# Optimization experiments

Measured on AMD Instinct MI355X. Metric: run time of the kernel, lower is better.

## Reference

```python
import jax, jax.numpy as jnp
import numpy as np

B, L, D = 1, 1024, 1024
NL = 4            # n_layers
N = 16            # d_state
DI = 2 * D        # d_inner (expand=2)
DTR = (D + 15) // 16  # dt_rank = ceil(d_model/16) = 64
K = 4             # depthwise conv kernel size
EPS = 1e-5


def setup_inputs() -> dict:
    key = jax.random.key(0)
    ks = jax.random.split(key, 8)
    s = lambda k, shp, sc: jax.random.normal(k, shp, jnp.float32) * sc
    x = s(ks[0], (B, L, D), 1.0)
    norm_w = jnp.ones((NL, D), jnp.float32)
    in_w = s(ks[1], (NL, 2 * DI, D), D ** -0.5)          # in_proj (no bias)
    conv_w = s(ks[2], (NL, DI, K), 0.5)                   # depthwise conv1d weight
    conv_b = s(ks[3], (NL, DI), 0.02)                     # conv1d bias
    xproj_w = s(ks[4], (NL, DTR + 2 * N, DI), DI ** -0.5) # x_proj (no bias)
    dt_w = s(ks[5], (NL, DI, DTR), DTR ** -0.5)           # dt_proj weight
    dt_b = jnp.full((NL, DI), 0.1, jnp.float32)           # dt_proj bias (positive-ish delta)
    A_log = jnp.log(jnp.tile(jnp.arange(1, N + 1, dtype=jnp.float32), (NL, DI, 1)))  # [NL, DI, N]
    D_skip = jnp.ones((NL, DI), jnp.float32)
    out_w = s(ks[6], (NL, D, DI), DI ** -0.5)             # out_proj (no bias)
    return dict(x=x, norm_w=norm_w, in_w=in_w, conv_w=conv_w, conv_b=conv_b,
                xproj_w=xproj_w, dt_w=dt_w, dt_b=dt_b, A_log=A_log,
                D_skip=D_skip, out_w=out_w)


def _rmsnorm(x, w):
    return x * jax.lax.rsqrt(jnp.mean(x * x, axis=-1, keepdims=True) + EPS) * w


def _causal_depthwise_conv(u, w, b):
    # u: [B, L, DI], w: [DI, K], b: [DI]; causal (left pad K-1)
    up = jnp.pad(u, ((0, 0), (K - 1, 0), (0, 0)))
    y = b
    for k in range(K):
        y = y + up[:, k:k + L, :] * w[:, k]
    return y


def _selective_scan(dA, dBu, C):
    # dA, dBu: [B, L, DI, N]; C: [B, L, N]
    def step(h, inp):
        a, bu, c = inp
        h = a * h + bu                       # [B, DI, N]
        y = jnp.einsum('bdn,bn->bd', h, c)   # [B, DI]
        return h, y
    h0 = jnp.zeros((dA.shape[0], DI, N), dA.dtype)
    _, ys = jax.lax.scan(step, h0, (dA.transpose(1, 0, 2, 3),
                                    dBu.transpose(1, 0, 2, 3),
                                    C.transpose(1, 0, 2)))
    return ys.transpose(1, 0, 2)             # [B, L, DI]


def _mamba_block(x, p):
    norm_w, in_w, conv_w, conv_b, xproj_w, dt_w, dt_b, A_log, D_skip, out_w = p
    xn = _rmsnorm(x, norm_w)
    xz = jnp.einsum('bld,ed->ble', xn, in_w)             # [B, L, 2*DI]
    u, z = jnp.split(xz, 2, axis=-1)
    u = jax.nn.silu(_causal_depthwise_conv(u, conv_w, conv_b))
    x_dbl = jnp.einsum('bld,ed->ble', u, xproj_w)        # [B, L, DTR+2N]
    dt_r, Bt, Ct = jnp.split(x_dbl, [DTR, DTR + N], axis=-1)
    delta = jax.nn.softplus(jnp.einsum('blr,dr->bld', dt_r, dt_w) + dt_b)  # [B, L, DI]
    A = -jnp.exp(A_log)                                  # [DI, N]
    dA = jnp.exp(delta[..., None] * A)                   # [B, L, DI, N]
    dBu = delta[..., None] * Bt[:, :, None, :] * u[..., None]
    y = _selective_scan(dA, dBu, Ct) + u * D_skip        # [B, L, DI]
    y = y * jax.nn.silu(z)
    return x + jnp.einsum('ble,de->bld', y, out_w)       # residual


def reference(x, norm_w, in_w, conv_w, conv_b, xproj_w, dt_w, dt_b, A_log, D_skip, out_w):
    params = (norm_w, in_w, conv_w, conv_b, xproj_w, dt_w, dt_b, A_log, D_skip, out_w)
    out, _ = jax.lax.scan(lambda h, p: (_mamba_block(h, p), None), x, params)
    return out
```

## Files before the change

### kernel.cpp

```cpp
#include <hip/hip_runtime.h>
#include <hip/hip_bf16.h>
#include <stdint.h>

#define L 1024
#define D 1024
#define NLAYER 4
#define NSTATE 16
#define DI 2048
#define DTR 64
#define KCONV 4
#define XD 96
#define NC 64
#define CT 16
#define KSPLIT 8
#define OSPLIT 4
#define BK 32
#define DIST 4

typedef __attribute__((ext_vector_type(8))) short short8;
typedef __attribute__((ext_vector_type(4))) float floatx4;

__device__ __forceinline__ float siluf(float x) { return x / (1.f + __expf(-x)); }

__device__ __forceinline__ unsigned short f2bf(float x) {
    __hip_bfloat16 b = __float2bfloat16(x);
    return *reinterpret_cast<unsigned short*>(&b);
}

__device__ __forceinline__ short8 pack8(floatx4 a, floatx4 b) {
    short8 o;
    o[0] = (short)f2bf(a.x); o[1] = (short)f2bf(a.y);
    o[2] = (short)f2bf(a.z); o[3] = (short)f2bf(a.w);
    o[4] = (short)f2bf(b.x); o[5] = (short)f2bf(b.y);
    o[6] = (short)f2bf(b.z); o[7] = (short)f2bf(b.w);
    return o;
}

#define BARRIER_NODRAIN() asm volatile("s_waitcnt lgkmcnt(0)\n\ts_barrier" ::: "memory")

__global__ __launch_bounds__(256) void rmsnorm_kernel(const float* __restrict__ x,
                                                      const float* __restrict__ w,
                                                      __hip_bfloat16* __restrict__ out) {
    int row = blockIdx.x;
    const float* xr = x + (size_t)row * D;
    float v[4];
    float s = 0.f;
#pragma unroll
    for (int i = 0; i < 4; ++i) {
        v[i] = xr[threadIdx.x + i * 256];
        s += v[i] * v[i];
    }
#pragma unroll
    for (int off = 32; off > 0; off >>= 1) s += __shfl_xor(s, off, 64);
    __shared__ float red[4];
    int wave = threadIdx.x >> 6;
    if ((threadIdx.x & 63) == 0) red[wave] = s;
    __syncthreads();
    float tot = red[0] + red[1] + red[2] + red[3];
    float inv = rsqrtf(tot * (1.f / D) + 1e-5f);
#pragma unroll
    for (int i = 0; i < 4; ++i) {
        int c = threadIdx.x + i * 256;
        out[(size_t)row * D + c] = __float2bfloat16(v[i] * inv * w[c]);
    }
}

template <int EPI, int ITERS>
__global__ __launch_bounds__(256, 2) void gemm_pipe(
    const __hip_bfloat16* __restrict__ A, int lda,
    const float* __restrict__ Bw, int ldb, int Brows,
    float* __restrict__ C, int ldc, int Nvalid,
    long zstride, const float* __restrict__ bias) {
    __shared__ __align__(16) __hip_bfloat16 As[2][128 * BK];
    __shared__ __align__(16) __hip_bfloat16 Bs[2][64 * BK];
    int tid = threadIdx.x;
    int wave = tid >> 6, lane = tid & 63;

    int gxy = gridDim.x * gridDim.y;
    int total = gxy * gridDim.z;
    int flat = (blockIdx.z * gridDim.y + blockIdx.y) * gridDim.x + blockIdx.x;
    int bm, bn, bz;
    if ((total & 7) == 0) {
        int lid = (flat & 7) * (total >> 3) + (flat >> 3);
        bz = lid / gxy;
        int rem = lid - bz * gxy;
        bn = rem / gridDim.y;
        bm = rem - bn * gridDim.y;
    } else {
        bm = blockIdx.y; bn = blockIdx.x; bz = blockIdx.z;
    }

    int m0 = bm * 128, n0 = bn * 64;
    int k_base = bz * (ITERS * BK);
    C += (long)bz * zstride;
    int wr = wave >> 1, wc = wave & 1;
    int srow = lane >> 2, scol = (lane & 3) * 8;
    int q = lane >> 4, r = lane & 15;

    floatx4 acc[4][2] = {};

    const __hip_bfloat16* gA0 = A + (long)(m0 + wave * 32 + srow) * lda + scol + k_base;
    const __hip_bfloat16* gA1 = gA0 + (long)16 * lda;
    int bnrow = n0 + wave * 16 + srow;
    const float* gB = Bw + (long)bnrow * ldb + scol + k_base;
    bool bok = bnrow < Brows;

    short8 qa0[DIST], qa1[DIST];
    floatx4 qb0[DIST] = {}, qb1[DIST] = {};

    auto ld = [&](int j) {
        int k0 = j * BK;
        int s = j & (DIST - 1);
        qa0[s] = *(const short8*)(gA0 + k0);
        qa1[s] = *(const short8*)(gA1 + k0);
        if (bok) {
            qb0[s] = *(const floatx4*)(gB + k0);
            qb1[s] = *(const floatx4*)(gB + k0 + 4);
        }
    };
    auto wrstage = [&](int j) {
        int p = j & 1, s = j & (DIST - 1);
        *(short8*)(&As[p][(wave * 32 + srow) * BK + scol]) = qa0[s];
        *(short8*)(&As[p][(wave * 32 + 16 + srow) * BK + scol]) = qa1[s];
        *(short8*)(&Bs[p][(wave * 16 + srow) * BK + scol]) = pack8(qb0[s], qb1[s]);
    };

#pragma unroll
    for (int j = 0; j < DIST; ++j)
        if (j < ITERS) ld(j);
    wrstage(0);

#pragma unroll
    for (int k = 0; k < ITERS; ++k) {
        BARRIER_NODRAIN();
        if (k + DIST < ITERS) ld(k + DIST);
        if (k + 1 < ITERS) wrstage(k + 1);
        const short* Ap = (const short*)As[k & 1];
        const short* Bp = (const short*)Bs[k & 1];
        short8 af[4], bfr[2];
#pragma unroll
        for (int i = 0; i < 4; ++i)
            af[i] = *(const short8*)(Ap + (wr * 64 + i * 16 + r) * BK + q * 8);
#pragma unroll
        for (int j = 0; j < 2; ++j)
            bfr[j] = *(const short8*)(Bp + (wc * 32 + j * 16 + r) * BK + q * 8);
#pragma unroll
        for (int i = 0; i < 4; ++i)
#pragma unroll
            for (int j = 0; j < 2; ++j)
                acc[i][j] = __builtin_amdgcn_mfma_f32_16x16x32_bf16(af[i], bfr[j], acc[i][j], 0, 0, 0);
    }

#pragma unroll
    for (int i = 0; i < 4; ++i) {
        int mrow = m0 + wr * 64 + i * 16 + q * 4;
#pragma unroll
        for (int j = 0; j < 2; ++j) {
            int ncol = n0 + wc * 32 + j * 16 + r;
            if (ncol < Nvalid) {
#pragma unroll
                for (int rr = 0; rr < 4; ++rr) {
                    float v = acc[i][j][rr];
                    int m = mrow + rr;
                    if (EPI == 1) {
                        v += bias[ncol];
                        v = v > 20.f ? v : log1pf(__expf(v));
                    }
                    C[(long)m * ldc + ncol] = v;
                }
            }
        }
    }
}

template <int ITERS>
__global__ __launch_bounds__(256, 1) void gemm128(
    const __hip_bfloat16* __restrict__ A, int lda,
    const float* __restrict__ Bw, int ldb, int Brows,
    float* __restrict__ C, int ldc,
    long zstride) {
    __shared__ __align__(16) __hip_bfloat16 As[2][128 * BK];
    __shared__ __align__(16) __hip_bfloat16 Bs[2][128 * BK];
    int tid = threadIdx.x;
    int wave = tid >> 6, lane = tid & 63;

    int gxy = gridDim.x * gridDim.y;
    int total = gxy * gridDim.z;
    int flat = (blockIdx.z * gridDim.y + blockIdx.y) * gridDim.x + blockIdx.x;
    int bm, bn, bz;
    if ((total & 7) == 0) {
        int lid = (flat & 7) * (total >> 3) + (flat >> 3);
        bz = lid / gxy;
        int rem = lid - bz * gxy;
        bn = rem / gridDim.y;
        bm = rem - bn * gridDim.y;
    } else {
        bm = blockIdx.y; bn = blockIdx.x; bz = blockIdx.z;
    }

    int m0 = bm * 128, n0 = bn * 128;
    int k_base = bz * (ITERS * BK);
    C += (long)bz * zstride;
    int wr = wave >> 1, wc = wave & 1;
    int srow = lane >> 2, scol = (lane & 3) * 8;
    int q = lane >> 4, r = lane & 15;

    floatx4 acc[4][4] = {};

    const __hip_bfloat16* gA0 = A + (long)(m0 + wave * 32 + srow) * lda + scol + k_base;
    const __hip_bfloat16* gA1 = gA0 + (long)16 * lda;
    int bn0 = n0 + wave * 32 + srow;
    const float* gB0 = Bw + (long)bn0 * ldb + scol + k_base;
    const float* gB1 = gB0 + (long)16 * ldb;
    bool bok0 = bn0 < Brows, bok1 = (bn0 + 16) < Brows;

    short8 qa0[DIST], qa1[DIST];
    floatx4 qb0[DIST] = {}, qb1[DIST] = {}, qb2[DIST] = {}, qb3[DIST] = {};

    auto ld = [&](int j) {
        int k0 = j * BK;
        int s = j & (DIST - 1);
        qa0[s] = *(const short8*)(gA0 + k0);
        qa1[s] = *(const short8*)(gA1 + k0);
        if (bok0) {
            qb0[s] = *(const floatx4*)(gB0 + k0);
            qb1[s] = *(const floatx4*)(gB0 + k0 + 4);
        }
        if (bok1) {
            qb2[s] = *(const floatx4*)(gB1 + k0);
            qb3[s] = *(const floatx4*)(gB1 + k0 + 4);
        }
    };
    auto wrstage = [&](int j) {
        int p = j & 1, s = j & (DIST - 1);
        *(short8*)(&As[p][(wave * 32 + srow) * BK + scol]) = qa0[s];
        *(short8*)(&As[p][(wave * 32 + 16 + srow) * BK + scol]) = qa1[s];
        *(short8*)(&Bs[p][(wave * 32 + srow) * BK + scol]) = pack8(qb0[s], qb1[s]);
        *(short8*)(&Bs[p][(wave * 32 + 16 + srow) * BK + scol]) = pack8(qb2[s], qb3[s]);
    };

#pragma unroll
    for (int j = 0; j < DIST; ++j)
        if (j < ITERS) ld(j);
    wrstage(0);

#pragma unroll
    for (int k = 0; k < ITERS; ++k) {
        BARRIER_NODRAIN();
        if (k + DIST < ITERS) ld(k + DIST);
        if (k + 1 < ITERS) wrstage(k + 1);
        const short* Ap = (const short*)As[k & 1];
        const short* Bp = (const short*)Bs[k & 1];
        short8 af[4], bfr[4];
#pragma unroll
        for (int i = 0; i < 4; ++i)
            af[i] = *(const short8*)(Ap + (wr * 64 + i * 16 + r) * BK + q * 8);
#pragma unroll
        for (int j = 0; j < 4; ++j)
            bfr[j] = *(const short8*)(Bp + (wc * 64 + j * 16 + r) * BK + q * 8);
#pragma unroll
        for (int i = 0; i < 4; ++i)
#pragma unroll
            for (int j = 0; j < 4; ++j)
                acc[i][j] = __builtin_amdgcn_mfma_f32_16x16x32_bf16(af[i], bfr[j], acc[i][j], 0, 0, 0);
    }

#pragma unroll
    for (int i = 0; i < 4; ++i) {
        int mrow = m0 + wr * 64 + i * 16 + q * 4;
#pragma unroll
        for (int j = 0; j < 4; ++j) {
            int ncol = n0 + wc * 64 + j * 16 + r;
#pragma unroll
            for (int rr = 0; rr < 4; ++rr)
                C[(long)(mrow + rr) * ldc + ncol] = acc[i][j][rr];
        }
    }
}

template <int NPART, bool NORM>
__global__ __launch_bounds__(256) void reduce_kernel(const float* __restrict__ part2,
                                                     const float* __restrict__ xin,
                                                     const float* __restrict__ nw,
                                                     float* __restrict__ out,
                                                     __hip_bfloat16* __restrict__ xn) {
    int row = blockIdx.x;
    const float* xr = xin + (size_t)row * D;
    float v[4];
    float ss = 0.f;
#pragma unroll
    for (int i = 0; i < 4; ++i) {
        int c = threadIdx.x + i * 256;
        float s = xr[c];
#pragma unroll
        for (int p = 0; p < NPART; ++p)
            s += part2[(size_t)p * L * D + (size_t)row * D + c];
        v[i] = s;
        out[(size_t)row * D + c] = s;
        ss += s * s;
    }
    if (NORM) {
#pragma unroll
        for (int off = 32; off > 0; off >>= 1) ss += __shfl_xor(ss, off, 64);
        __shared__ float red[4];
        int wave = threadIdx.x >> 6;
        if ((threadIdx.x & 63) == 0) red[wave] = ss;
        __syncthreads();
        float inv = rsqrtf((red[0] + red[1] + red[2] + red[3]) * (1.f / D) + 1e-5f);
#pragma unroll
        for (int i = 0; i < 4; ++i) {
            int c = threadIdx.x + i * 256;
            xn[(size_t)row * D + c] = __float2bfloat16(v[i] * inv * nw[c]);
        }
    }
}

__global__ __launch_bounds__(256) void conv_silu_kernel(const float* __restrict__ xz,
                                                        const float* __restrict__ cw,
                                                        const float* __restrict__ cb,
                                                        __hip_bfloat16* __restrict__ u) {
    int idx = blockIdx.x * 256 + threadIdx.x;
    int d = idx & (DI - 1);
    int t = idx >> 11;
    float acc = cb[d];
#pragma unroll
    for (int k = 0; k < KCONV; ++k) {
        int tk = t - (KCONV - 1) + k;
        if (tk >= 0) acc += xz[(size_t)tk * (2 * DI) + d] * cw[d * KCONV + k];
    }
    u[idx] = __float2bfloat16(siluf(acc));
}

__global__ __launch_bounds__(256) void xred_kernel(const float* __restrict__ part,
                                                   __hip_bfloat16* __restrict__ xdbl_bf,
                                                   float* __restrict__ xdblBC) {
    int i = blockIdx.x * 256 + threadIdx.x;
    int t = i / XD, col = i - t * XD;
    float s = 0.f;
#pragma unroll
    for (int sp = 0; sp < KSPLIT; ++sp) s += part[(size_t)sp * L * XD + i];
    if (col < DTR) xdbl_bf[(size_t)t * DTR + col] = __float2bfloat16(s);
    else xdblBC[(size_t)t * 32 + (col - DTR)] = s;
}

__global__ __launch_bounds__(256) void scanA_kernel(const float* __restrict__ delta,
                                                    const __hip_bfloat16* __restrict__ u,
                                                    const float* __restrict__ xdblBC,
                                                    const float* __restrict__ Alog,
                                                    float* __restrict__ Ach,
                                                    float* __restrict__ Bch) {
    int d = blockIdx.x * 256 + threadIdx.x;
    int c = blockIdx.y;
    __shared__ __align__(16) float Bsh[CT * NSTATE];
    int tt0 = threadIdx.x >> 4, c0 = threadIdx.x & 15;
    Bsh[threadIdx.x] = xdblBC[(size_t)(c * CT + tt0) * 32 + c0];
    __syncthreads();

    float aval[NSTATE];
    const float4* Al4 = (const float4*)(Alog + (size_t)d * NSTATE);
#pragma unroll
    for (int n4 = 0; n4 < 4; ++n4) {
        float4 t = Al4[n4];
        aval[n4 * 4 + 0] = -__expf(t.x);
        aval[n4 * 4 + 1] = -__expf(t.y);
        aval[n4 * 4 + 2] = -__expf(t.z);
        aval[n4 * 4 + 3] = -__expf(t.w);
    }
    float h[NSTATE], ap[NSTATE];
#pragma unroll
    for (int n = 0; n < NSTATE; ++n) { h[n] = 0.f; ap[n] = 1.f; }

    for (int tt = 0; tt < CT; ++tt) {
        int t = c * CT + tt;
        float dl = delta[(size_t)t * DI + d];
        float uu = __bfloat162float(u[(size_t)t * DI + d]);
        float du = dl * uu;
        const float4* Bv = (const float4*)(Bsh + tt * NSTATE);
#pragma unroll
        for (int n4 = 0; n4 < 4; ++n4) {
            float4 b = Bv[n4];
            float bb[4] = {b.x, b.y, b.z, b.w};
#pragma unroll
            for (int k = 0; k < 4; ++k) {
                int n = n4 * 4 + k;
                float a = __expf(dl * aval[n]);
                h[n] = a * h[n] + du * bb[k];
                ap[n] *= a;
            }
        }
    }
    float4* Ao = (float4*)(Ach + ((size_t)c * DI + d) * NSTATE);
    float4* Bo = (float4*)(Bch + ((size_t)c * DI + d) * NSTATE);
#pragma unroll
    for (int n4 = 0; n4 < 4; ++n4) {
        Ao[n4] = make_float4(ap[n4 * 4], ap[n4 * 4 + 1], ap[n4 * 4 + 2], ap[n4 * 4 + 3]);
        Bo[n4] = make_float4(h[n4 * 4], h[n4 * 4 + 1], h[n4 * 4 + 2], h[n4 * 4 + 3]);
    }
}

__global__ __launch_bounds__(256) void scanB_kernel(float* __restrict__ Ach,
                                                    const float* __restrict__ Bch) {
    long i = blockIdx.x * 256 + threadIdx.x;
    const long S = (long)DI * NSTATE;
    constexpr int P = 8;
    float ab[P], bb[P];
#pragma unroll
    for (int j = 0; j < P; ++j) {
        ab[j] = Ach[(long)j * S + i];
        bb[j] = Bch[(long)j * S + i];
    }
    float h = 0.f;
#pragma unroll
    for (int c = 0; c < NC; ++c) {
        float a = ab[c & (P - 1)];
        float b = bb[c & (P - 1)];
        Ach[(long)c * S + i] = h;
        if (c + P < NC) {
            ab[c & (P - 1)] = Ach[(long)(c + P) * S + i];
            bb[c & (P - 1)] = Bch[(long)(c + P) * S + i];
        }
        h = a * h + b;
    }
}

__global__ __launch_bounds__(256) void scanC_kernel(const float* __restrict__ delta,
                                                    const __hip_bfloat16* __restrict__ u,
                                                    const float* __restrict__ xdblBC,
                                                    const float* __restrict__ Alog,
                                                    const float* __restrict__ Hin,
                                                    const float* __restrict__ xz,
                                                    const float* __restrict__ Dskip,
                                                    __hip_bfloat16* __restrict__ yg) {
    int d = blockIdx.x * 256 + threadIdx.x;
    int c = blockIdx.y;
    __shared__ __align__(16) float Bsh[CT * NSTATE];
    __shared__ __align__(16) float Csh[CT * NSTATE];
    int tt0 = threadIdx.x >> 4, c0 = threadIdx.x & 15;
    Bsh[threadIdx.x] = xdblBC[(size_t)(c * CT + tt0) * 32 + c0];
    Csh[threadIdx.x] = xdblBC[(size_t)(c * CT + tt0) * 32 + 16 + c0];
    __syncthreads();

    float aval[NSTATE];
    const float4* Al4 = (const float4*)(Alog + (size_t)d * NSTATE);
#pragma unroll
    for (int n4 = 0; n4 < 4; ++n4) {
        float4 t = Al4[n4];
        aval[n4 * 4 + 0] = -__expf(t.x);
        aval[n4 * 4 + 1] = -__expf(t.y);
        aval[n4 * 4 + 2] = -__expf(t.z);
        aval[n4 * 4 + 3] = -__expf(t.w);
    }
    float h[NSTATE];
    const float4* Hi = (const float4*)(Hin + ((size_t)c * DI + d) * NSTATE);
#pragma unroll
    for (int n4 = 0; n4 < 4; ++n4) {
        float4 t = Hi[n4];
        h[n4 * 4 + 0] = t.x; h[n4 * 4 + 1] = t.y; h[n4 * 4 + 2] = t.z; h[n4 * 4 + 3] = t.w;
    }
    float dsk = Dskip[d];

    for (int tt = 0; tt < CT; ++tt) {
        int t = c * CT + tt;
        float dl = delta[(size_t)t * DI + d];
        float uu = __bfloat162float(u[(size_t)t * DI + d]);
        float du = dl * uu;
        const float4* Bv = (const float4*)(Bsh + tt * NSTATE);
        const float4* Cv = (const float4*)(Csh + tt * NSTATE);
        float y = 0.f;
#pragma unroll
        for (int n4 = 0; n4 < 4; ++n4) {
            float4 b = Bv[n4];
            float4 cc = Cv[n4];
            float bb[4] = {b.x, b.y, b.z, b.w};
            float cv[4] = {cc.x, cc.y, cc.z, cc.w};
#pragma unroll
            for (int k = 0; k < 4; ++k) {
                int n = n4 * 4 + k;
                float a = __expf(dl * aval[n]);
                h[n] = a * h[n] + du * bb[k];
                y += h[n] * cv[k];
            }
        }
        float z = xz[(size_t)t * (2 * DI) + DI + d];
        yg[(size_t)t * DI + d] = __float2bfloat16((y + uu * dsk) * siluf(z));
    }
}

extern "C" void kernel_launch(void* const* d_in, const int* in_sizes, int n_in,
                              void* d_out, int out_size, void* d_ws, size_t ws_size,
                              hipStream_t stream) {
    const float* x      = (const float*)d_in[0];
    const float* norm_w = (const float*)d_in[1];
    const float* in_w   = (const float*)d_in[2];
    const float* conv_w = (const float*)d_in[3];
    const float* conv_b = (const float*)d_in[4];
    const float* xproj_w= (const float*)d_in[5];
    const float* dt_w   = (const float*)d_in[6];
    const float* dt_b   = (const float*)d_in[7];
    const float* A_log  = (const float*)d_in[8];
    const float* D_skip = (const float*)d_in[9];
    const float* out_w  = (const float*)d_in[10];
    float* out = (float*)d_out;

    uint8_t* wp = (uint8_t*)d_ws;
    auto alloc = [&](size_t bytes) {
        uint8_t* p = wp;
        wp += (bytes + 255) & ~(size_t)255;
        return p;
    };
    __hip_bfloat16* xn_bf   = (__hip_bfloat16*)alloc((size_t)L * D * 2);
    float*          xz      = (float*)alloc((size_t)L * 2 * DI * 4);
    __hip_bfloat16* u_bf    = (__hip_bfloat16*)alloc((size_t)L * DI * 2);
    float*          part    = (float*)alloc((size_t)KSPLIT * L * XD * 4);
    __hip_bfloat16* xdbl_bf = (__hip_bfloat16*)alloc((size_t)L * DTR * 2);
    float*          xdblBC  = (float*)alloc((size_t)L * 32 * 4);
    float*          delta   = (float*)alloc((size_t)L * DI * 4);
    __hip_bfloat16* yg_bf   = (__hip_bfloat16*)alloc((size_t)L * DI * 2);
    float*          part2   = (float*)alloc((size_t)OSPLIT * L * D * 4);
    float*          Ach     = (float*)alloc((size_t)NC * DI * NSTATE * 4);
    float*          Bch     = (float*)alloc((size_t)NC * DI * NSTATE * 4);

    rmsnorm_kernel<<<L, 256, 0, stream>>>(x, norm_w, xn_bf);

    for (int l = 0; l < NLAYER; ++l) {
        const float* xin = (l == 0) ? x : out;

        gemm128<32><<<dim3(4096 / 128, L / 128, 1), 256, 0, stream>>>(
            xn_bf, D, in_w + (size_t)l * 4096 * 1024, D, 4096,
            xz, 4096, 0);

        conv_silu_kernel<<<L * DI / 256, 256, 0, stream>>>(
            xz, conv_w + (size_t)l * DI * KCONV, conv_b + (size_t)l * DI, u_bf);

        gemm_pipe<0, 8><<<dim3(2, L / 128, KSPLIT), 256, 0, stream>>>(
            u_bf, DI, xproj_w + (size_t)l * 96 * 2048, DI, 96,
            part, XD, XD, (long)L * XD, nullptr);
        xred_kernel<<<(L * XD) / 256, 256, 0, stream>>>(part, xdbl_bf, xdblBC);

        gemm_pipe<1, 2><<<dim3(2048 / 64, L / 128, 1), 256, 0, stream>>>(
            xdbl_bf, DTR, dt_w + (size_t)l * 2048 * 64, DTR, 2048,
            delta, DI, DI, 0, dt_b + (size_t)l * DI);

        scanA_kernel<<<dim3(DI / 256, NC), 256, 0, stream>>>(
            delta, u_bf, xdblBC, A_log + (size_t)l * DI * NSTATE, Ach, Bch);
        scanB_kernel<<<(DI * NSTATE) / 256, 256, 0, stream>>>(Ach, Bch);
        scanC_kernel<<<dim3(DI / 256, NC), 256, 0, stream>>>(
            delta, u_bf, xdblBC, A_log + (size_t)l * DI * NSTATE, Ach, xz,
            D_skip + (size_t)l * DI, yg_bf);

        gemm128<16><<<dim3(1024 / 128, L / 128, OSPLIT), 256, 0, stream>>>(
            yg_bf, DI, out_w + (size_t)l * 1024 * 2048, DI, 1024,
            part2, D, (long)L * D);

        if (l < NLAYER - 1)
            reduce_kernel<OSPLIT, true><<<L, 256, 0, stream>>>(
                part2, xin, norm_w + (size_t)(l + 1) * D, out, xn_bf);
        else
            reduce_kernel<OSPLIT, false><<<L, 256, 0, stream>>>(
                part2, xin, nullptr, out, nullptr);
    }
}
```

Before: 598.7 us.

## Replace split-K partial buffers and reduction kernels with atomic accumulation

The x_proj and out_proj split-K GEMMs now atomically add into a single output buffer instead of writing partials that a separate reduce kernel sums. The residual is seeded by copying x into out during the first rmsnorm, and the x_dbl buffer is zeroed inside the conv kernel. The dt_proj GEMM reads the fp32 x_dbl directly and converts it to bf16 in-kernel, which removes the xred kernel. This saves launches and partial-buffer traffic, but fp32 atomics make the summation order nondeterministic, and KSPLIT doubles to 16.

```diff
diff --git a/kernel.cpp b/kernel.cpp
--- a/kernel.cpp
+++ b/kernel.cpp
@@ -12,7 +12,7 @@
 #define XD 96
 #define NC 64
 #define CT 16
-#define KSPLIT 8
+#define KSPLIT 16
 #define OSPLIT 4
 #define BK 32
 #define DIST 4
@@ -38,9 +38,11 @@
 
 #define BARRIER_NODRAIN() asm volatile("s_waitcnt lgkmcnt(0)\n\ts_barrier" ::: "memory")
 
+template <bool COPYOUT>
 __global__ __launch_bounds__(256) void rmsnorm_kernel(const float* __restrict__ x,
                                                       const float* __restrict__ w,
-                                                      __hip_bfloat16* __restrict__ out) {
+                                                      __hip_bfloat16* __restrict__ xn,
+                                                      float* __restrict__ outcpy) {
     int row = blockIdx.x;
     const float* xr = x + (size_t)row * D;
     float v[4];
@@ -61,16 +63,17 @@
 #pragma unroll
     for (int i = 0; i < 4; ++i) {
         int c = threadIdx.x + i * 256;
-        out[(size_t)row * D + c] = __float2bfloat16(v[i] * inv * w[c]);
-    }
-}
-
-template <int EPI, int ITERS>
+        xn[(size_t)row * D + c] = __float2bfloat16(v[i] * inv * w[c]);
+        if (COPYOUT) outcpy[(size_t)row * D + c] = v[i];
+    }
+}
+
+template <int EPI, int ITERS, bool AF32, int QD>
 __global__ __launch_bounds__(256, 2) void gemm_pipe(
-    const __hip_bfloat16* __restrict__ A, int lda,
+    const void* __restrict__ Aptr, int lda,
     const float* __restrict__ Bw, int ldb, int Brows,
     float* __restrict__ C, int ldc, int Nvalid,
-    long zstride, const float* __restrict__ bias) {
+    const float* __restrict__ bias) {
     __shared__ __align__(16) __hip_bfloat16 As[2][128 * BK];
     __shared__ __align__(16) __hip_bfloat16 Bs[2][64 * BK];
     int tid = threadIdx.x;
@@ -92,48 +95,68 @@
 
     int m0 = bm * 128, n0 = bn * 64;
     int k_base = bz * (ITERS * BK);
-    C += (long)bz * zstride;
     int wr = wave >> 1, wc = wave & 1;
     int srow = lane >> 2, scol = (lane & 3) * 8;
     int q = lane >> 4, r = lane & 15;
 
     floatx4 acc[4][2] = {};
 
-    const __hip_bfloat16* gA0 = A + (long)(m0 + wave * 32 + srow) * lda + scol + k_base;
-    const __hip_bfloat16* gA1 = gA0 + (long)16 * lda;
+    int arow0 = m0 + wave * 32 + srow;
+    const __hip_bfloat16* gA0 = nullptr; const __hip_bfloat16* gA1 = nullptr;
+    const float* gAf0 = nullptr; const float* gAf1 = nullptr;
+    if (AF32) {
+        gAf0 = (const float*)Aptr + (long)arow0 * lda + scol + k_base;
+        gAf1 = gAf0 + (long)16 * lda;
+    } else {
+        gA0 = (const __hip_bfloat16*)Aptr + (long)arow0 * lda + scol + k_base;
+        gA1 = gA0 + (long)16 * lda;
+    }
     int bnrow = n0 + wave * 16 + srow;
     const float* gB = Bw + (long)bnrow * ldb + scol + k_base;
     bool bok = bnrow < Brows;
 
-    short8 qa0[DIST], qa1[DIST];
-    floatx4 qb0[DIST] = {}, qb1[DIST] = {};
+    short8 qa0[QD], qa1[QD];
+    floatx4 qaf[AF32 ? QD : 1][4];
+    floatx4 qb0[QD] = {}, qb1[QD] = {};
 
     auto ld = [&](int j) {
         int k0 = j * BK;
-        int s = j & (DIST - 1);
-        qa0[s] = *(const short8*)(gA0 + k0);
-        qa1[s] = *(const short8*)(gA1 + k0);
+        int s = j & (QD - 1);
+        if (AF32) {
+            qaf[s][0] = *(const floatx4*)(gAf0 + k0);
+            qaf[s][1] = *(const floatx4*)(gAf0 + k0 + 4);
+            qaf[s][2] = *(const floatx4*)(gAf1 + k0);
+            qaf[s][3] = *(const floatx4*)(gAf1 + k0 + 4);
+        } else {
+            qa0[s] = *(const short8*)(gA0 + k0);
+            qa1[s] = *(const short8*)(gA1 + k0);
+        }
         if (bok) {
             qb0[s] = *(const floatx4*)(gB + k0);
             qb1[s] = *(const floatx4*)(gB + k0 + 4);
         }
     };
     auto wrstage = [&](int j) {
-        int p = j & 1, s = j & (DIST - 1);
-        *(short8*)(&As[p][(wave * 32 + srow) * BK + scol]) = qa0[s];
-        *(short8*)(&As[p][(wave * 32 + 16 + srow) * BK + scol]) = qa1[s];
+        int p = j & 1, s = j & (QD - 1);
+        if (AF32) {
+            *(short8*)(&As[p][(wave * 32 + srow) * BK + scol]) = pack8(qaf[s][0], qaf[s][1]);
+            *(short8*)(&As[p][(wave * 32 + 16 + srow) * BK + scol]) = pack8(qaf[s][2], qaf[s][3]);
+        } else {
+            *(short8*)(&As[p][(wave * 32 + srow) * BK + scol]) = qa0[s];
+            *(short8*)(&As[p][(wave * 32 + 16 + srow) * BK + scol]) = qa1[s];
+        }
         *(short8*)(&Bs[p][(wave * 16 + srow) * BK + scol]) = pack8(qb0[s], qb1[s]);
     };
 
 #pragma unroll
-    for (int j = 0; j < DIST; ++j)
+    for (int j = 0; j < QD; ++j)
         if (j < ITERS) ld(j);
     wrstage(0);
 
 #pragma unroll
     for (int k = 0; k < ITERS; ++k) {
         BARRIER_NODRAIN();
-        if (k + DIST < ITERS) ld(k + DIST);
+        if (k + QD < ITERS) ld(k + QD);
         if (k + 1 < ITERS) wrstage(k + 1);
         const short* Ap = (const short*)As[k & 1];
         const short* Bp = (const short*)Bs[k & 1];
@@ -166,19 +189,19 @@
                         v += bias[ncol];
                         v = v > 20.f ? v : log1pf(__expf(v));
                     }
-                    C[(long)m * ldc + ncol] = v;
+                    if (EPI == 2) atomicAdd(&C[(long)m * ldc + ncol], v);
+                    else C[(long)m * ldc + ncol] = v;
                 }
             }
         }
     }
 }
 
-template <int ITERS>
+template <int ITERS, int EPI>
 __global__ __launch_bounds__(256, 1) void gemm128(
     const __hip_bfloat16* __restrict__ A, int lda,
     const float* __restrict__ Bw, int ldb, int Brows,
-    float* __restrict__ C, int ldc,
-    long zstride) {
+    float* __restrict__ C, int ldc) {
     __shared__ __align__(16) __hip_bfloat16 As[2][128 * BK];
     __shared__ __align__(16) __hip_bfloat16 Bs[2][128 * BK];
     int tid = threadIdx.x;
@@ -200,7 +223,6 @@
 
     int m0 = bm * 128, n0 = bn * 128;
     int k_base = bz * (ITERS * BK);
-    C += (long)bz * zstride;
     int wr = wave >> 1, wc = wave & 1;
     int srow = lane >> 2, scol = (lane & 3) * 8;
     int q = lane >> 4, r = lane & 15;
@@ -272,45 +294,10 @@
         for (int j = 0; j < 4; ++j) {
             int ncol = n0 + wc * 64 + j * 16 + r;
 #pragma unroll
-            for (int rr = 0; rr < 4; ++rr)
-                C[(long)(mrow + rr) * ldc + ncol] = acc[i][j][rr];
-        }
-    }
-}
-
-template <int NPART, bool NORM>
-__global__ __launch_bounds__(256) void reduce_kernel(const float* __restrict__ part2,
-                                                     const float* __restrict__ xin,
-                                                     const float* __restrict__ nw,
-                                                     float* __restrict__ out,
-                                                     __hip_bfloat16* __restrict__ xn) {
-    int row = blockIdx.x;
-    const float* xr = xin + (size_t)row * D;
-    float v[4];
-    float ss = 0.f;
-#pragma unroll
-    for (int i = 0; i < 4; ++i) {
-        int c = threadIdx.x + i * 256;
-        float s = xr[c];
-#pragma unroll
-        for (int p = 0; p < NPART; ++p)
-            s += part2[(size_t)p * L * D + (size_t)row * D + c];
-        v[i] = s;
-        out[(size_t)row * D + c] = s;
-        ss += s * s;
-    }
-    if (NORM) {
-#pragma unroll
-        for (int off = 32; off > 0; off >>= 1) ss += __shfl_xor(ss, off, 64);
-        __shared__ float red[4];
-        int wave = threadIdx.x >> 6;
-        if ((threadIdx.x & 63) == 0) red[wave] = ss;
-        __syncthreads();
-        float inv = rsqrtf((red[0] + red[1] + red[2] + red[3]) * (1.f / D) + 1e-5f);
-#pragma unroll
-        for (int i = 0; i < 4; ++i) {
-            int c = threadIdx.x + i * 256;
-            xn[(size_t)row * D + c] = __float2bfloat16(v[i] * inv * nw[c]);
+            for (int rr = 0; rr < 4; ++rr) {
+                if (EPI == 2) atomicAdd(&C[(long)(mrow + rr) * ldc + ncol], acc[i][j][rr]);
+                else C[(long)(mrow + rr) * ldc + ncol] = acc[i][j][rr];
+            }
         }
     }
 }
@@ -318,8 +305,10 @@
 __global__ __launch_bounds__(256) void conv_silu_kernel(const float* __restrict__ xz,
                                                         const float* __restrict__ cw,
                                                         const float* __restrict__ cb,
-                                                        __hip_bfloat16* __restrict__ u) {
+                                                        __hip_bfloat16* __restrict__ u,
+                                                        float* __restrict__ xdbl96) {
     int idx = blockIdx.x * 256 + threadIdx.x;
+    if (blockIdx.x < (L * XD) / 256) xdbl96[idx] = 0.f;
     int d = idx & (DI - 1);
     int t = idx >> 11;
     float acc = cb[d];
@@ -331,21 +320,9 @@
     u[idx] = __float2bfloat16(siluf(acc));
 }
 
-__global__ __launch_bounds__(256) void xred_kernel(const float* __restrict__ part,
-                                                   __hip_bfloat16* __restrict__ xdbl_bf,
-                                                   float* __restrict__ xdblBC) {
-    int i = blockIdx.x * 256 + threadIdx.x;
-    int t = i / XD, col = i - t * XD;
-    float s = 0.f;
-#pragma unroll
-    for (int sp = 0; sp < KSPLIT; ++sp) s += part[(size_t)sp * L * XD + i];
-    if (col < DTR) xdbl_bf[(size_t)t * DTR + col] = __float2bfloat16(s);
-    else xdblBC[(size_t)t * 32 + (col - DTR)] = s;
-}
-
 __global__ __launch_bounds__(256) void scanA_kernel(const float* __restrict__ delta,
                                                     const __hip_bfloat16* __restrict__ u,
-                                                    const float* __restrict__ xdblBC,
+                                                    const float* __restrict__ xdbl96,
                                                     const float* __restrict__ Alog,
                                                     float* __restrict__ Ach,
                                                     float* __restrict__ Bch) {
@@ -353,7 +330,7 @@
     int c = blockIdx.y;
     __shared__ __align__(16) float Bsh[CT * NSTATE];
     int tt0 = threadIdx.x >> 4, c0 = threadIdx.x & 15;
-    Bsh[threadIdx.x] = xdblBC[(size_t)(c * CT + tt0) * 32 + c0];
+    Bsh[threadIdx.x] = xdbl96[(size_t)(c * CT + tt0) * XD + DTR + c0];
     __syncthreads();
 
     float aval[NSTATE];
@@ -425,7 +402,7 @@
 
 __global__ __launch_bounds__(256) void scanC_kernel(const float* __restrict__ delta,
                                                     const __hip_bfloat16* __restrict__ u,
-                                                    const float* __restrict__ xdblBC,
+                                                    const float* __restrict__ xdbl96,
                                                     const float* __restrict__ Alog,
                                                     const float* __restrict__ Hin,
                                                     const float* __restrict__ xz,
@@ -436,8 +413,8 @@
     __shared__ __align__(16) float Bsh[CT * NSTATE];
     __shared__ __align__(16) float Csh[CT * NSTATE];
     int tt0 = threadIdx.x >> 4, c0 = threadIdx.x & 15;
-    Bsh[threadIdx.x] = xdblBC[(size_t)(c * CT + tt0) * 32 + c0];
-    Csh[threadIdx.x] = xdblBC[(size_t)(c * CT + tt0) * 32 + 16 + c0];
+    Bsh[threadIdx.x] = xdbl96[(size_t)(c * CT + tt0) * XD + DTR + c0];
+    Csh[threadIdx.x] = xdbl96[(size_t)(c * CT + tt0) * XD + DTR + 16 + c0];
     __syncthreads();
 
     float aval[NSTATE];
@@ -511,52 +488,41 @@
     __hip_bfloat16* xn_bf   = (__hip_bfloat16*)alloc((size_t)L * D * 2);
     float*          xz      = (float*)alloc((size_t)L * 2 * DI * 4);
     __hip_bfloat16* u_bf    = (__hip_bfloat16*)alloc((size_t)L * DI * 2);
-    float*          part    = (float*)alloc((size_t)KSPLIT * L * XD * 4);
-    __hip_bfloat16* xdbl_bf = (__hip_bfloat16*)alloc((size_t)L * DTR * 2);
-    float*          xdblBC  = (float*)alloc((size_t)L * 32 * 4);
+    float*          xdbl96  = (float*)alloc((size_t)L * XD * 4);
     float*          delta   = (float*)alloc((size_t)L * DI * 4);
     __hip_bfloat16* yg_bf   = (__hip_bfloat16*)alloc((size_t)L * DI * 2);
-    float*          part2   = (float*)alloc((size_t)OSPLIT * L * D * 4);
     float*          Ach     = (float*)alloc((size_t)NC * DI * NSTATE * 4);
     float*          Bch     = (float*)alloc((size_t)NC * DI * NSTATE * 4);
 
-    rmsnorm_kernel<<<L, 256, 0, stream>>>(x, norm_w, xn_bf);
+    rmsnorm_kernel<true><<<L, 256, 0, stream>>>(x, norm_w, xn_bf, out);
 
     for (int l = 0; l < NLAYER; ++l) {
-        const float* xin = (l == 0) ? x : out;
-
-        gemm128<32><<<dim3(4096 / 128, L / 128, 1), 256, 0, stream>>>(
-            xn_bf, D, in_w + (size_t)l * 4096 * 1024, D, 4096,
-            xz, 4096, 0);
+        gemm128<32, 0><<<dim3(4096 / 128, L / 128, 1), 256, 0, stream>>>(
+            xn_bf, D, in_w + (size_t)l * 4096 * 1024, D, 4096, xz, 4096);
 
         conv_silu_kernel<<<L * DI / 256, 256, 0, stream>>>(
-            xz, conv_w + (size_t)l * DI * KCONV, conv_b + (size_t)l * DI, u_bf);
-
-        gemm_pipe<0, 8><<<dim3(2, L / 128, KSPLIT), 256, 0, stream>>>(
+            xz, conv_w + (size_t)l * DI * KCONV, conv_b + (size_t)l * DI, u_bf, xdbl96);
+
+        gemm_pipe<2, 2048 / (KSPLIT * BK), false, 4><<<dim3(2, L / 128, KSPLIT), 256, 0, stream>>>(
             u_bf, DI, xproj_w + (size_t)l * 96 * 2048, DI, 96,
-            part, XD, XD, (long)L * XD, nullptr);
-        xred_kernel<<<(L * XD) / 256, 256, 0, stream>>>(part, xdbl_bf, xdblBC);
-
-        gemm_pipe<1, 2><<<dim3(2048 / 64, L / 128, 1), 256, 0, stream>>>(
-            xdbl_bf, DTR, dt_w + (size_t)l * 2048 * 64, DTR, 2048,
-            delta, DI, DI, 0, dt_b + (size_t)l * DI);
+            xdbl96, XD, XD, nullptr);
+
+        gemm_pipe<1, 2, true, 2><<<dim3(2048 / 64, L / 128, 1), 256, 0, stream>>>(
+            xdbl96, XD, dt_w + (size_t)l * 2048 * 64, DTR, 2048,
+            delta, DI, DI, dt_b + (size_t)l * DI);
 
         scanA_kernel<<<dim3(DI / 256, NC), 256, 0, stream>>>(
-            delta, u_bf, xdblBC, A_log + (size_t)l * DI * NSTATE, Ach, Bch);
+            delta, u_bf, xdbl96, A_log + (size_t)l * DI * NSTATE, Ach, Bch);
         scanB_kernel<<<(DI * NSTATE) / 256, 256, 0, stream>>>(Ach, Bch);
         scanC_kernel<<<dim3(DI / 256, NC), 256, 0, stream>>>(
-            delta, u_bf, xdblBC, A_log + (size_t)l * DI * NSTATE, Ach, xz,
+            delta, u_bf, xdbl96, A_log + (size_t)l * DI * NSTATE, Ach, xz,
             D_skip + (size_t)l * DI, yg_bf);
 
-        gemm128<16><<<dim3(1024 / 128, L / 128, OSPLIT), 256, 0, stream>>>(
-            yg_bf, DI, out_w + (size_t)l * 1024 * 2048, DI, 1024,
-            part2, D, (long)L * D);
+        gemm128<2048 / (OSPLIT * BK), 2><<<dim3(1024 / 128, L / 128, OSPLIT), 256, 0, stream>>>(
+            yg_bf, DI, out_w + (size_t)l * 1024 * 2048, DI, 1024, out, D);
 
         if (l < NLAYER - 1)
-            reduce_kernel<OSPLIT, true><<<L, 256, 0, stream>>>(
-                part2, xin, norm_w + (size_t)(l + 1) * D, out, xn_bf);
-        else
-            reduce_kernel<OSPLIT, false><<<L, 256, 0, stream>>>(
-                part2, xin, nullptr, out, nullptr);
-    }
-}
+            rmsnorm_kernel<false><<<L, 256, 0, stream>>>(
+                out, norm_w + (size_t)(l + 1) * D, xn_bf, nullptr);
+    }
+}
```

Result: slower. 618.4 us (+3.3%).

## Fuse conv+SiLU into x_proj GEMM and fold split-K reduction into consumers

Applied to the files above, without the earlier changes.

The causal depthwise conv and SiLU now run inside the A-operand load of the x_proj GEMM, and only the bn==0 blocks write u to global for later use. The separate xred kernel is removed: the dt_proj GEMM sums the KSPLIT partials as it loads its A tile, and the scan kernels sum the B/C partials when filling shared memory. This cuts two launches and several intermediate buffers. In exchange the conv is recomputed per N-block (two blocks per tile), and the split-K partial sums are reread by many blocks.

```diff
diff --git a/kernel.cpp b/kernel.cpp
--- a/kernel.cpp
+++ b/kernel.cpp
@@ -40,7 +40,7 @@
 
 __global__ __launch_bounds__(256) void rmsnorm_kernel(const float* __restrict__ x,
                                                       const float* __restrict__ w,
-                                                      __hip_bfloat16* __restrict__ out) {
+                                                      __hip_bfloat16* __restrict__ xn) {
     int row = blockIdx.x;
     const float* xr = x + (size_t)row * D;
     float v[4];
@@ -56,21 +56,20 @@
     int wave = threadIdx.x >> 6;
     if ((threadIdx.x & 63) == 0) red[wave] = s;
     __syncthreads();
-    float tot = red[0] + red[1] + red[2] + red[3];
-    float inv = rsqrtf(tot * (1.f / D) + 1e-5f);
+    float inv = rsqrtf((red[0] + red[1] + red[2] + red[3]) * (1.f / D) + 1e-5f);
 #pragma unroll
     for (int i = 0; i < 4; ++i) {
         int c = threadIdx.x + i * 256;
-        out[(size_t)row * D + c] = __float2bfloat16(v[i] * inv * w[c]);
-    }
-}
-
-template <int EPI, int ITERS>
+        xn[(size_t)row * D + c] = __float2bfloat16(v[i] * inv * w[c]);
+    }
+}
+
+template <int EPI, bool ASUM, int ITERS, int QD>
 __global__ __launch_bounds__(256, 2) void gemm_pipe(
-    const __hip_bfloat16* __restrict__ A, int lda,
+    const void* __restrict__ Aptr, int lda, long astride,
     const float* __restrict__ Bw, int ldb, int Brows,
-    float* __restrict__ C, int ldc, int Nvalid,
-    long zstride, const float* __restrict__ bias) {
+    float* __restrict__ C, int ldc, int Nvalid, long zstride,
+    const float* __restrict__ bias) {
     __shared__ __align__(16) __hip_bfloat16 As[2][128 * BK];
     __shared__ __align__(16) __hip_bfloat16 Bs[2][64 * BK];
     int tid = threadIdx.x;
@@ -99,41 +98,70 @@
 
     floatx4 acc[4][2] = {};
 
-    const __hip_bfloat16* gA0 = A + (long)(m0 + wave * 32 + srow) * lda + scol + k_base;
-    const __hip_bfloat16* gA1 = gA0 + (long)16 * lda;
+    int arow0 = m0 + wave * 32 + srow;
+    const __hip_bfloat16* gA0 = nullptr; const __hip_bfloat16* gA1 = nullptr;
+    const float* gAf0 = nullptr; const float* gAf1 = nullptr;
+    if (ASUM) {
+        gAf0 = (const float*)Aptr + (long)arow0 * lda + scol + k_base;
+        gAf1 = gAf0 + (long)16 * lda;
+    } else {
+        gA0 = (const __hip_bfloat16*)Aptr + (long)arow0 * lda + scol + k_base;
+        gA1 = gA0 + (long)16 * lda;
+    }
     int bnrow = n0 + wave * 16 + srow;
     const float* gB = Bw + (long)bnrow * ldb + scol + k_base;
     bool bok = bnrow < Brows;
 
-    short8 qa0[DIST], qa1[DIST];
-    floatx4 qb0[DIST] = {}, qb1[DIST] = {};
+    short8 qa0[QD], qa1[QD];
+    floatx4 qaf[ASUM ? QD : 1][4];
+    floatx4 qb0[QD] = {}, qb1[QD] = {};
 
     auto ld = [&](int j) {
         int k0 = j * BK;
-        int s = j & (DIST - 1);
-        qa0[s] = *(const short8*)(gA0 + k0);
-        qa1[s] = *(const short8*)(gA1 + k0);
+        int s = j & (QD - 1);
+        if (ASUM) {
+            floatx4 t0 = *(const floatx4*)(gAf0 + k0);
+            floatx4 t1 = *(const floatx4*)(gAf0 + k0 + 4);
+            floatx4 t2 = *(const floatx4*)(gAf1 + k0);
+            floatx4 t3 = *(const floatx4*)(gAf1 + k0 + 4);
+#pragma unroll
+            for (int sp = 1; sp < KSPLIT; ++sp) {
+                t0 += *(const floatx4*)(gAf0 + sp * astride + k0);
+                t1 += *(const floatx4*)(gAf0 + sp * astride + k0 + 4);
+                t2 += *(const floatx4*)(gAf1 + sp * astride + k0);
+                t3 += *(const floatx4*)(gAf1 + sp * astride + k0 + 4);
+            }
+            qaf[s][0] = t0; qaf[s][1] = t1; qaf[s][2] = t2; qaf[s][3] = t3;
+        } else {
+            qa0[s] = *(const short8*)(gA0 + k0);
+            qa1[s] = *(const short8*)(gA1 + k0);
+        }
         if (bok) {
             qb0[s] = *(const floatx4*)(gB + k0);
             qb1[s] = *(const floatx4*)(gB + k0 + 4);
         }
     };
     auto wrstage = [&](int j) {
-        int p = j & 1, s = j & (DIST - 1);
-        *(short8*)(&As[p][(wave * 32 + srow) * BK + scol]) = qa0[s];
-        *(short8*)(&As[p][(wave * 32 + 16 + srow) * BK + scol]) = qa1[s];
+        int p = j & 1, s = j & (QD - 1);
+        if (ASUM) {
+            *(short8*)(&As[p][(wave * 32 + srow) * BK + scol]) = pack8(qaf[s][0], qaf[s][1]);
+            *(short8*)(&As[p][(wave * 32 + 16 + srow) * BK + scol]) = pack8(qaf[s][2], qaf[s][3]);
+        } else {
+            *(short8*)(&As[p][(wave * 32 + srow) * BK + scol]) = qa0[s];
+            *(short8*)(&As[p][(wave * 32 + 16 + srow) * BK + scol]) = qa1[s];
+        }
         *(short8*)(&Bs[p][(wave * 16 + srow) * BK + scol]) = pack8(qb0[s], qb1[s]);
     };
 
 #pragma unroll
-    for (int j = 0; j < DIST; ++j)
+    for (int j = 0; j < QD; ++j)
         if (j < ITERS) ld(j);
     wrstage(0);
 
 #pragma unroll
     for (int k = 0; k < ITERS; ++k) {
         BARRIER_NODRAIN();
-        if (k + DIST < ITERS) ld(k + DIST);
+        if (k + QD < ITERS) ld(k + QD);
         if (k + 1 < ITERS) wrstage(k + 1);
         const short* Ap = (const short*)As[k & 1];
         const short* Bp = (const short*)Bs[k & 1];
@@ -173,14 +201,15 @@
     }
 }
 
-template <int ITERS>
-__global__ __launch_bounds__(256, 1) void gemm128(
-    const __hip_bfloat16* __restrict__ A, int lda,
+template <int ITERS, int QD>
+__global__ __launch_bounds__(256, 2) void xproj_conv_kernel(
+    const float* __restrict__ xz,
+    const float* __restrict__ cw, const float* __restrict__ cb,
     const float* __restrict__ Bw, int ldb, int Brows,
-    float* __restrict__ C, int ldc,
-    long zstride) {
+    float* __restrict__ C, int ldc, int Nvalid, long zstride,
+    __hip_bfloat16* __restrict__ uout) {
     __shared__ __align__(16) __hip_bfloat16 As[2][128 * BK];
-    __shared__ __align__(16) __hip_bfloat16 Bs[2][128 * BK];
+    __shared__ __align__(16) __hip_bfloat16 Bs[2][64 * BK];
     int tid = threadIdx.x;
     int wave = tid >> 6, lane = tid & 63;
 
@@ -198,6 +227,137 @@
         bm = blockIdx.y; bn = blockIdx.x; bz = blockIdx.z;
     }
 
+    int m0 = bm * 128, n0 = bn * 64;
+    int k_base = bz * (ITERS * BK);
+    C += (long)bz * zstride;
+    int wr = wave >> 1, wc = wave & 1;
+    int srow = lane >> 2, scol = (lane & 3) * 8;
+    int q = lane >> 4, r = lane & 15;
+
+    floatx4 acc[4][2] = {};
+
+    int t0 = m0 + wave * 32 + srow;
+    int bnrow = n0 + wave * 16 + srow;
+    const float* gB = Bw + (long)bnrow * ldb + scol + k_base;
+    bool bok = bnrow < Brows;
+    bool uwr = (bn == 0);
+
+    short8 qa0[QD], qa1[QD];
+    floatx4 qb0[QD] = {}, qb1[QD] = {};
+
+    auto conv8 = [&](int t, int dcol, const floatx4* w, floatx4 cb0, floatx4 cb1) -> short8 {
+        float a[8] = {cb0[0], cb0[1], cb0[2], cb0[3], cb1[0], cb1[1], cb1[2], cb1[3]};
+#pragma unroll
+        for (int k = 0; k < KCONV; ++k) {
+            int tr = t - (KCONV - 1) + k;
+            if (tr >= 0) {
+                floatx4 x0 = *(const floatx4*)(xz + (size_t)tr * 4096 + dcol);
+                floatx4 x1 = *(const floatx4*)(xz + (size_t)tr * 4096 + dcol + 4);
+#pragma unroll
+                for (int i = 0; i < 4; ++i) {
+                    a[i] += x0[i] * w[i][k];
+                    a[4 + i] += x1[i] * w[4 + i][k];
+                }
+            }
+        }
+        short8 o;
+#pragma unroll
+        for (int i = 0; i < 8; ++i) o[i] = (short)f2bf(siluf(a[i]));
+        return o;
+    };
+
+    auto ld = [&](int j) {
+        int k0 = j * BK;
+        int s = j & (QD - 1);
+        int dcol = k_base + k0 + scol;
+        floatx4 w[8];
+#pragma unroll
+        for (int i = 0; i < 8; ++i) w[i] = *(const floatx4*)(cw + (dcol + i) * KCONV);
+        floatx4 cb0 = *(const floatx4*)(cb + dcol);
+        floatx4 cb1 = *(const floatx4*)(cb + dcol + 4);
+        qa0[s] = conv8(t0, dcol, w, cb0, cb1);
+        qa1[s] = conv8(t0 + 16, dcol, w, cb0, cb1);
+        if (uwr) {
+            *(short8*)(uout + (size_t)t0 * DI + dcol) = qa0[s];
+            *(short8*)(uout + (size_t)(t0 + 16) * DI + dcol) = qa1[s];
+        }
+        if (bok) {
+            qb0[s] = *(const floatx4*)(gB + k0);
+            qb1[s] = *(const floatx4*)(gB + k0 + 4);
+        }
+    };
+    auto wrstage = [&](int j) {
+        int p = j & 1, s = j & (QD - 1);
+        *(short8*)(&As[p][(wave * 32 + srow) * BK + scol]) = qa0[s];
+        *(short8*)(&As[p][(wave * 32 + 16 + srow) * BK + scol]) = qa1[s];
+        *(short8*)(&Bs[p][(wave * 16 + srow) * BK + scol]) = pack8(qb0[s], qb1[s]);
+    };
+
+#pragma unroll
+    for (int j = 0; j < QD; ++j)
+        if (j < ITERS) ld(j);
+    wrstage(0);
+
+#pragma unroll
+    for (int k = 0; k < ITERS; ++k) {
+        BARRIER_NODRAIN();
+        if (k + QD < ITERS) ld(k + QD);
+        if (k + 1 < ITERS) wrstage(k + 1);
+        const short* Ap = (const short*)As[k & 1];
+        const short* Bp = (const short*)Bs[k & 1];
+        short8 af[4], bfr[2];
+#pragma unroll
+        for (int i = 0; i < 4; ++i)
+            af[i] = *(const short8*)(Ap + (wr * 64 + i * 16 + r) * BK + q * 8);
+#pragma unroll
+        for (int j = 0; j < 2; ++j)
+            bfr[j] = *(const short8*)(Bp + (wc * 32 + j * 16 + r) * BK + q * 8);
+#pragma unroll
+        for (int i = 0; i < 4; ++i)
+#pragma unroll
+            for (int j = 0; j < 2; ++j)
+                acc[i][j] = __builtin_amdgcn_mfma_f32_16x16x32_bf16(af[i], bfr[j], acc[i][j], 0, 0, 0);
+    }
+
+#pragma unroll
+    for (int i = 0; i < 4; ++i) {
+        int mrow = m0 + wr * 64 + i * 16 + q * 4;
+#pragma unroll
+        for (int j = 0; j < 2; ++j) {
+            int ncol = n0 + wc * 32 + j * 16 + r;
+            if (ncol < Nvalid) {
+#pragma unroll
+                for (int rr = 0; rr < 4; ++rr)
+                    C[(long)(mrow + rr) * ldc + ncol] = acc[i][j][rr];
+            }
+        }
+    }
+}
+
+template <int ITERS>
+__global__ __launch_bounds__(256, 1) void gemm128(
+    const __hip_bfloat16* __restrict__ A, int lda,
+    const float* __restrict__ Bw, int ldb, int Brows,
+    float* __restrict__ C, int ldc, long zstride) {
+    __shared__ __align__(16) __hip_bfloat16 As[2][128 * BK];
+    __shared__ __align__(16) __hip_bfloat16 Bs[2][128 * BK];
+    int tid = threadIdx.x;
+    int wave = tid >> 6, lane = tid & 63;
+
+    int gxy = gridDim.x * gridDim.y;
+    int total = gxy * gridDim.z;
+    int flat = (blockIdx.z * gridDim.y + blockIdx.y) * gridDim.x + blockIdx.x;
+    int bm, bn, bz;
+    if ((total & 7) == 0) {
+        int lid = (flat & 7) * (total >> 3) + (flat >> 3);
+        bz = lid / gxy;
+        int rem = lid - bz * gxy;
+        bn = rem / gridDim.y;
+        bm = rem - bn * gridDim.y;
+    } else {
+        bm = blockIdx.y; bn = blockIdx.x; bz = blockIdx.z;
+    }
+
     int m0 = bm * 128, n0 = bn * 128;
     int k_base = bz * (ITERS * BK);
     C += (long)bz * zstride;
@@ -315,45 +475,23 @@
     }
 }
 
-__global__ __launch_bounds__(256) void conv_silu_kernel(const float* __restrict__ xz,
-                                                        const float* __restrict__ cw,
-                                                        const float* __restrict__ cb,
-                                                        __hip_bfloat16* __restrict__ u) {
-    int idx = blockIdx.x * 256 + threadIdx.x;
-    int d = idx & (DI - 1);
-    int t = idx >> 11;
-    float acc = cb[d];
-#pragma unroll
-    for (int k = 0; k < KCONV; ++k) {
-        int tk = t - (KCONV - 1) + k;
-        if (tk >= 0) acc += xz[(size_t)tk * (2 * DI) + d] * cw[d * KCONV + k];
-    }
-    u[idx] = __float2bfloat16(siluf(acc));
-}
-
-__global__ __launch_bounds__(256) void xred_kernel(const float* __restrict__ part,
-                                                   __hip_bfloat16* __restrict__ xdbl_bf,
-                                                   float* __restrict__ xdblBC) {
-    int i = blockIdx.x * 256 + threadIdx.x;
-    int t = i / XD, col = i - t * XD;
-    float s = 0.f;
-#pragma unroll
-    for (int sp = 0; sp < KSPLIT; ++sp) s += part[(size_t)sp * L * XD + i];
-    if (col < DTR) xdbl_bf[(size_t)t * DTR + col] = __float2bfloat16(s);
-    else xdblBC[(size_t)t * 32 + (col - DTR)] = s;
-}
-
 __global__ __launch_bounds__(256) void scanA_kernel(const float* __restrict__ delta,
                                                     const __hip_bfloat16* __restrict__ u,
-                                                    const float* __restrict__ xdblBC,
+                                                    const float* __restrict__ part,
                                                     const float* __restrict__ Alog,
                                                     float* __restrict__ Ach,
                                                     float* __restrict__ Bch) {
     int d = blockIdx.x * 256 + threadIdx.x;
     int c = blockIdx.y;
     __shared__ __align__(16) float Bsh[CT * NSTATE];
-    int tt0 = threadIdx.x >> 4, c0 = threadIdx.x & 15;
-    Bsh[threadIdx.x] = xdblBC[(size_t)(c * CT + tt0) * 32 + c0];
+    {
+        int tt = threadIdx.x >> 4, col = threadIdx.x & 15;
+        float sum = 0.f;
+#pragma unroll
+        for (int sp = 0; sp < KSPLIT; ++sp)
+            sum += part[(size_t)sp * L * XD + (size_t)(c * CT + tt) * XD + DTR + col];
+        Bsh[threadIdx.x] = sum;
+    }
     __syncthreads();
 
     float aval[NSTATE];
@@ -425,7 +563,7 @@
 
 __global__ __launch_bounds__(256) void scanC_kernel(const float* __restrict__ delta,
                                                     const __hip_bfloat16* __restrict__ u,
-                                                    const float* __restrict__ xdblBC,
+                                                    const float* __restrict__ part,
                                                     const float* __restrict__ Alog,
                                                     const float* __restrict__ Hin,
                                                     const float* __restrict__ xz,
@@ -435,9 +573,15 @@
     int c = blockIdx.y;
     __shared__ __align__(16) float Bsh[CT * NSTATE];
     __shared__ __align__(16) float Csh[CT * NSTATE];
-    int tt0 = threadIdx.x >> 4, c0 = threadIdx.x & 15;
-    Bsh[threadIdx.x] = xdblBC[(size_t)(c * CT + tt0) * 32 + c0];
-    Csh[threadIdx.x] = xdblBC[(size_t)(c * CT + tt0) * 32 + 16 + c0];
+    for (int s2 = threadIdx.x; s2 < CT * 32; s2 += 256) {
+        int tt = s2 >> 5, col = s2 & 31;
+        float sum = 0.f;
+#pragma unroll
+        for (int sp = 0; sp < KSPLIT; ++sp)
+            sum += part[(size_t)sp * L * XD + (size_t)(c * CT + tt) * XD + DTR + col];
+        if (col < 16) Bsh[tt * NSTATE + col] = sum;
+        else          Csh[tt * NSTATE + (col - 16)] = sum;
+    }
     __syncthreads();
 
     float aval[NSTATE];
@@ -512,8 +656,6 @@
     float*          xz      = (float*)alloc((size_t)L * 2 * DI * 4);
     __hip_bfloat16* u_bf    = (__hip_bfloat16*)alloc((size_t)L * DI * 2);
     float*          part    = (float*)alloc((size_t)KSPLIT * L * XD * 4);
-    __hip_bfloat16* xdbl_bf = (__hip_bfloat16*)alloc((size_t)L * DTR * 2);
-    float*          xdblBC  = (float*)alloc((size_t)L * 32 * 4);
     float*          delta   = (float*)alloc((size_t)L * DI * 4);
     __hip_bfloat16* yg_bf   = (__hip_bfloat16*)alloc((size_t)L * DI * 2);
     float*          part2   = (float*)alloc((size_t)OSPLIT * L * D * 4);
@@ -526,29 +668,25 @@
         const float* xin = (l == 0) ? x : out;
 
         gemm128<32><<<dim3(4096 / 128, L / 128, 1), 256, 0, stream>>>(
-            xn_bf, D, in_w + (size_t)l * 4096 * 1024, D, 4096,
-            xz, 4096, 0);
-
-        conv_silu_kernel<<<L * DI / 256, 256, 0, stream>>>(
-            xz, conv_w + (size_t)l * DI * KCONV, conv_b + (size_t)l * DI, u_bf);
-
-        gemm_pipe<0, 8><<<dim3(2, L / 128, KSPLIT), 256, 0, stream>>>(
-            u_bf, DI, xproj_w + (size_t)l * 96 * 2048, DI, 96,
-            part, XD, XD, (long)L * XD, nullptr);
-        xred_kernel<<<(L * XD) / 256, 256, 0, stream>>>(part, xdbl_bf, xdblBC);
-
-        gemm_pipe<1, 2><<<dim3(2048 / 64, L / 128, 1), 256, 0, stream>>>(
-            xdbl_bf, DTR, dt_w + (size_t)l * 2048 * 64, DTR, 2048,
+            xn_bf, D, in_w + (size_t)l * 4096 * 1024, D, 4096, xz, 4096, 0);
+
+        xproj_conv_kernel<2048 / (KSPLIT * BK), 2><<<dim3(2, L / 128, KSPLIT), 256, 0, stream>>>(
+            xz, conv_w + (size_t)l * DI * KCONV, conv_b + (size_t)l * DI,
+            xproj_w + (size_t)l * 96 * 2048, DI, 96,
+            part, XD, XD, (long)L * XD, u_bf);
+
+        gemm_pipe<1, true, 2, 2><<<dim3(2048 / 64, L / 128, 1), 256, 0, stream>>>(
+            part, XD, (long)L * XD, dt_w + (size_t)l * 2048 * 64, DTR, 2048,
             delta, DI, DI, 0, dt_b + (size_t)l * DI);
 
         scanA_kernel<<<dim3(DI / 256, NC), 256, 0, stream>>>(
-            delta, u_bf, xdblBC, A_log + (size_t)l * DI * NSTATE, Ach, Bch);
+            delta, u_bf, part, A_log + (size_t)l * DI * NSTATE, Ach, Bch);
         scanB_kernel<<<(DI * NSTATE) / 256, 256, 0, stream>>>(Ach, Bch);
         scanC_kernel<<<dim3(DI / 256, NC), 256, 0, stream>>>(
-            delta, u_bf, xdblBC, A_log + (size_t)l * DI * NSTATE, Ach, xz,
+            delta, u_bf, part, A_log + (size_t)l * DI * NSTATE, Ach, xz,
             D_skip + (size_t)l * DI, yg_bf);
 
-        gemm128<16><<<dim3(1024 / 128, L / 128, OSPLIT), 256, 0, stream>>>(
+        gemm128<2048 / (OSPLIT * BK)><<<dim3(1024 / 128, L / 128, OSPLIT), 256, 0, stream>>>(
             yg_bf, DI, out_w + (size_t)l * 1024 * 2048, DI, 1024,
             part2, D, (long)L * D);
 
```

Result: slower. 680.8 us (+13.7%).
